# Kernel tuning notes

Measured on AMD Instinct MI355X. Metric: run time of the kernel, lower is better.

The kernel has to match this reference:

```python
import jax, jax.numpy as jnp
import numpy as np

N, M, K = 4096, 256, 32
W_EPS = 1e-6


def _spd(key, n, k):
    # well-conditioned SPD precision matrices: A A^T / k + I
    a = jax.random.normal(key, (n, k, k), dtype=jnp.float32)
    return jnp.matmul(a, jnp.swapaxes(a, -1, -2)) / k + jnp.eye(k, dtype=jnp.float32)


def setup_inputs() -> dict:
    key = jax.random.key(0)
    k1, k2, k3, k4 = jax.random.split(key, 4)
    W = jax.random.uniform(k1, (N, M), dtype=jnp.float32)
    mu_s = jax.random.normal(k2, (N, K), dtype=jnp.float32)
    omega_child = _spd(k3, N, K)
    omega_parent = _spd(k4, M, K)
    return {"W": W, "mu_s": mu_s, "omega_child": omega_child, "omega_parent": omega_parent}


def reference(W, mu_s, omega_child, omega_parent):
    # mask out negligible memberships (original skips w < 1e-6)
    wT = W.T                                   # (M, N)
    mask = wT >= W_EPS
    w = jnp.where(mask, wT, 0.0)

    # v_i = inv(omega_child_i) @ mu_s_i  -> batched solve, (N, K)
    v = jnp.linalg.solve(omega_child, mu_s[..., None])[..., 0]

    # transported means: Omega_alpha @ v_i, (M, N, K)
    T = jnp.einsum('mkl,nl->mnk', omega_parent, v)

    Z = w.sum(-1)                              # (M,)
    Zs = jnp.maximum(Z, 1e-30)
    mu_bar = jnp.einsum('mn,mnk->mk', w, T) / Zs[:, None]
    diff = T - mu_bar[:, None, :]              # (M, N, K)
    var = jnp.einsum('mn,mnk->mk', w, diff * diff) / Zs[:, None]
    psi = var.sum(-1)                          # (M,)

    # clusters with fewer than 2 contributing agents get psi = 0
    count = mask.sum(-1)
    return jnp.where(count >= 2, psi, 0.0)
```

## Files before the change

kernel.cpp:

```cpp
#include <hip/hip_runtime.h>

constexpr int N_AG = 4096;
constexpr int M_CL = 256;
constexpr int KD   = 32;
constexpr float WEPS = 1e-6f;

constexpr int PART_STRIDE = 1088;
constexpr int VT_OFF = M_CL * 4 * PART_STRIDE;
constexpr int WT_OFF = VT_OFF + N_AG * KD;

typedef __attribute__((ext_vector_type(8))) short short8;
typedef __attribute__((ext_vector_type(4))) float f32x4;

__device__ __forceinline__ float rlane(float x, int l) {
    return __int_as_float(__builtin_amdgcn_readlane(__float_as_int(x), l));
}
__device__ __forceinline__ short8 mk8(unsigned a, unsigned b, unsigned c, unsigned d) {
    union { unsigned u[4]; short8 s; } x;
    x.u[0] = a; x.u[1] = b; x.u[2] = c; x.u[3] = d;
    return x.s;
}

#define ALL32(M) M(0) M(1) M(2) M(3) M(4) M(5) M(6) M(7) \
                 M(8) M(9) M(10) M(11) M(12) M(13) M(14) M(15) \
                 M(16) M(17) M(18) M(19) M(20) M(21) M(22) M(23) \
                 M(24) M(25) M(26) M(27) M(28) M(29) M(30) M(31)

#define DECL(I) float a##I, b##I;
#define LDA(I) a##I = (c < 32) ? oc[ia_ * 1024 + I * 32 + c] : mu[ia_ * 32 + I]; \
               b##I = (c < 32) ? oc[ib_ * 1024 + I * 32 + c] : mu[ib_ * 32 + I];
#define EL(I, J) if constexpr (I != J) { \
    const float fa##I = rlane(a##I, J); a##I = fmaf(-fa##I, a##J, a##I); \
    const float fb##I = rlane(b##I, J); b##I = fmaf(-fb##I, b##J, b##I); }
#define ELALL(J) EL(0,J) EL(1,J) EL(2,J) EL(3,J) EL(4,J) EL(5,J) EL(6,J) EL(7,J) \
                 EL(8,J) EL(9,J) EL(10,J) EL(11,J) EL(12,J) EL(13,J) EL(14,J) EL(15,J) \
                 EL(16,J) EL(17,J) EL(18,J) EL(19,J) EL(20,J) EL(21,J) EL(22,J) EL(23,J) \
                 EL(24,J) EL(25,J) EL(26,J) EL(27,J) EL(28,J) EL(29,J) EL(30,J) EL(31,J)
#define STEP(J) { \
    const float pa = rlane(a##J, J); const float pb = rlane(b##J, J); \
    const float qa = 1.0f / pa;      const float qb = 1.0f / pb; \
    a##J *= qa;                      b##J *= qb; \
    ELALL(J) }
#define OUTP(I) { const float xa = rlane(a##I, 32); const float xb = rlane(b##I, 32); \
    if (lane == I) { ova = xa; ovb = xb; } }

__global__ __launch_bounds__(256, 1) void solve_transpose_kernel(
        const float* __restrict__ oc, const float* __restrict__ mu,
        const float* __restrict__ W,
        float* __restrict__ vT, float* __restrict__ Wt) {
    __shared__ float res8[32][8];
    __shared__ float tb[32][33];

    const int t    = threadIdx.x;
    const int lane = t & 63;
    const int wv   = t >> 6;
    const int idx0 = blockIdx.x * 8;
    const int ia_  = idx0 + 2 * wv;
    const int ib_  = ia_ + 1;
    const int c = (lane < 32) ? lane : 32;

    ALL32(DECL)
    ALL32(LDA)
    ALL32(STEP)

    float ova = 0.0f, ovb = 0.0f;
    ALL32(OUTP)

    if (lane < 32) {
        res8[lane][2 * wv]     = ova;
        res8[lane][2 * wv + 1] = ovb;
    }
    __syncthreads();
    {
        const int k = t >> 3, j = t & 7;
        vT[(size_t)k * 4096 + idx0 + j] = res8[k][j];
    }

    const int x = t & 31, y = t >> 5;
    #pragma unroll
    for (int rep = 0; rep < 2; ++rep) {
        const int tile = blockIdx.x * 2 + rep;
        const int n0 = (tile & 127) * 32;
        const int m0 = (tile >> 7) * 32;
        __syncthreads();
        #pragma unroll
        for (int r = 0; r < 4; ++r) {
            const int n = y + 8 * r;
            const float w = W[(size_t)(n0 + n) * 256 + m0 + x];
            tb[n][x] = (w >= WEPS) ? w : 0.0f;
        }
        __syncthreads();
        #pragma unroll
        for (int r = 0; r < 4; ++r) {
            const int mm = y + 8 * r;
            Wt[(size_t)(m0 + mm) * 4096 + n0 + x] = tb[x][mm];
        }
    }
}

__global__ __launch_bounds__(256, 4) void partial_kernel(const float* __restrict__ Wt,
                                                         const float* __restrict__ vT,
                                                         float* __restrict__ wsout) {
    const int m = blockIdx.x >> 2;
    const int p = blockIdx.x & 3;
    const int t = threadIdx.x;
    const int lane = t & 63;
    const int wv   = t >> 6;

    __shared__ float swbuf[1024];
    __shared__ float sred[4 * 1024];
    __shared__ float red[256];
    __shared__ float s1buf[32];

    const float4 wv4 = reinterpret_cast<const float4*>(Wt + (size_t)m * 4096 + p * 1024)[t];
    const float zacc = wv4.x + wv4.y + wv4.z + wv4.w;
    const float cacc = (wv4.x >= WEPS ? 1.f : 0.f) + (wv4.y >= WEPS ? 1.f : 0.f)
                     + (wv4.z >= WEPS ? 1.f : 0.f) + (wv4.w >= WEPS ? 1.f : 0.f);
    reinterpret_cast<float4*>(swbuf)[t] =
        make_float4(sqrtf(wv4.x), sqrtf(wv4.y), sqrtf(wv4.z), sqrtf(wv4.w));
    if (t < 32) s1buf[t] = 0.0f;
    __syncthreads();

    const int a = lane & 15;
    const int g = lane >> 4;
    const int nl = wv * 256 + g * 8;

    const float4* pa4 = reinterpret_cast<const float4*>(vT + (size_t)a * 4096 + p * 1024 + nl);
    const float4* pb4 = reinterpret_cast<const float4*>(vT + (size_t)(a + 16) * 4096 + p * 1024 + nl);

    f32x4 Chh[4], Chl[4];
    #pragma unroll
    for (int q = 0; q < 4; ++q) {
        Chh[q] = (f32x4){0.f, 0.f, 0.f, 0.f};
        Chl[q] = (f32x4){0.f, 0.f, 0.f, 0.f};
    }
    float s1a = 0.0f, s1b = 0.0f;

    #pragma unroll 2
    for (int ch = 0; ch < 8; ++ch) {
        const float4 va0 = pa4[ch * 8];
        const float4 va1 = pa4[ch * 8 + 1];
        const float4 vb0 = pb4[ch * 8];
        const float4 vb1 = pb4[ch * 8 + 1];
        const float4 s0  = *reinterpret_cast<const float4*>(&swbuf[nl + ch * 32]);
        const float4 s1v = *reinterpret_cast<const float4*>(&swbuf[nl + ch * 32 + 4]);

        const float ua0 = va0.x * s0.x,  ua1 = va0.y * s0.y;
        const float ua2 = va0.z * s0.z,  ua3 = va0.w * s0.w;
        const float ua4 = va1.x * s1v.x, ua5 = va1.y * s1v.y;
        const float ua6 = va1.z * s1v.z, ua7 = va1.w * s1v.w;
        const float ub0 = vb0.x * s0.x,  ub1 = vb0.y * s0.y;
        const float ub2 = vb0.z * s0.z,  ub3 = vb0.w * s0.w;
        const float ub4 = vb1.x * s1v.x, ub5 = vb1.y * s1v.y;
        const float ub6 = vb1.z * s1v.z, ub7 = vb1.w * s1v.w;

        s1a += s0.x*ua0 + s0.y*ua1 + s0.z*ua2 + s0.w*ua3
             + s1v.x*ua4 + s1v.y*ua5 + s1v.z*ua6 + s1v.w*ua7;
        s1b += s0.x*ub0 + s0.y*ub1 + s0.z*ub2 + s0.w*ub3
             + s1v.x*ub4 + s1v.y*ub5 + s1v.z*ub6 + s1v.w*ub7;

        #define BITS(u) __float_as_uint(u)
        #define LOF(u) ((u) - __uint_as_float(BITS(u) & 0xFFFF0000u))
        const short8 h0 = mk8(
            __builtin_amdgcn_perm(BITS(ua1), BITS(ua0), 0x07060302u),
            __builtin_amdgcn_perm(BITS(ua3), BITS(ua2), 0x07060302u),
            __builtin_amdgcn_perm(BITS(ua5), BITS(ua4), 0x07060302u),
            __builtin_amdgcn_perm(BITS(ua7), BITS(ua6), 0x07060302u));
        const short8 h1 = mk8(
            __builtin_amdgcn_perm(BITS(ub1), BITS(ub0), 0x07060302u),
            __builtin_amdgcn_perm(BITS(ub3), BITS(ub2), 0x07060302u),
            __builtin_amdgcn_perm(BITS(ub5), BITS(ub4), 0x07060302u),
            __builtin_amdgcn_perm(BITS(ub7), BITS(ub6), 0x07060302u));
        const float la0 = LOF(ua0), la1 = LOF(ua1), la2 = LOF(ua2), la3 = LOF(ua3);
        const float la4 = LOF(ua4), la5 = LOF(ua5), la6 = LOF(ua6), la7 = LOF(ua7);
        const float lb0 = LOF(ub0), lb1 = LOF(ub1), lb2 = LOF(ub2), lb3 = LOF(ub3);
        const float lb4 = LOF(ub4), lb5 = LOF(ub5), lb6 = LOF(ub6), lb7 = LOF(ub7);
        const short8 l0 = mk8(
            __builtin_amdgcn_perm(BITS(la1), BITS(la0), 0x07060302u),
            __builtin_amdgcn_perm(BITS(la3), BITS(la2), 0x07060302u),
            __builtin_amdgcn_perm(BITS(la5), BITS(la4), 0x07060302u),
            __builtin_amdgcn_perm(BITS(la7), BITS(la6), 0x07060302u));
        const short8 l1 = mk8(
            __builtin_amdgcn_perm(BITS(lb1), BITS(lb0), 0x07060302u),
            __builtin_amdgcn_perm(BITS(lb3), BITS(lb2), 0x07060302u),
            __builtin_amdgcn_perm(BITS(lb5), BITS(lb4), 0x07060302u),
            __builtin_amdgcn_perm(BITS(lb7), BITS(lb6), 0x07060302u));
        #undef BITS
        #undef LOF

        Chh[0] = __builtin_amdgcn_mfma_f32_16x16x32_bf16(h0, h0, Chh[0], 0, 0, 0);
        Chh[1] = __builtin_amdgcn_mfma_f32_16x16x32_bf16(h0, h1, Chh[1], 0, 0, 0);
        Chh[2] = __builtin_amdgcn_mfma_f32_16x16x32_bf16(h1, h0, Chh[2], 0, 0, 0);
        Chh[3] = __builtin_amdgcn_mfma_f32_16x16x32_bf16(h1, h1, Chh[3], 0, 0, 0);
        Chl[0] = __builtin_amdgcn_mfma_f32_16x16x32_bf16(h0, l0, Chl[0], 0, 0, 0);
        Chl[1] = __builtin_amdgcn_mfma_f32_16x16x32_bf16(h0, l1, Chl[1], 0, 0, 0);
        Chl[2] = __builtin_amdgcn_mfma_f32_16x16x32_bf16(h1, l0, Chl[2], 0, 0, 0);
        Chl[3] = __builtin_amdgcn_mfma_f32_16x16x32_bf16(h1, l1, Chl[3], 0, 0, 0);
    }

    s1a += __shfl_xor(s1a, 16); s1a += __shfl_xor(s1a, 32);
    s1b += __shfl_xor(s1b, 16); s1b += __shfl_xor(s1b, 32);
    if (lane < 16) {
        atomicAdd(&s1buf[a], s1a);
        atomicAdd(&s1buf[a + 16], s1b);
    }

    float* rw = &sred[wv * 1024];
    #pragma unroll
    for (int q = 0; q < 4; ++q) {
        const int I = q >> 1, J = q & 1;
        #pragma unroll
        for (int r = 0; r < 4; ++r) {
            const int ar = I * 16 + (lane >> 4) * 4 + r;
            const int br = J * 16 + (lane & 15);
            rw[ar * 32 + br] = Chh[q][r] + Chl[q][r];
        }
    }
    __syncthreads();
    #pragma unroll
    for (int q = 0; q < 4; ++q) {
        const int I = q >> 1, J = q & 1;
        #pragma unroll
        for (int r = 0; r < 4; ++r) {
            const int ar = I * 16 + (lane >> 4) * 4 + r;
            const int br = J * 16 + (lane & 15);
            rw[br * 32 + ar] += Chl[q][r];
        }
    }
    __syncthreads();

    const size_t base = (size_t)(m * 4 + p) * PART_STRIDE;
    float o0 = 0.f, o1 = 0.f, o2 = 0.f, o3 = 0.f;
    #pragma unroll
    for (int ww = 0; ww < 4; ++ww) {
        const float4 x = *reinterpret_cast<const float4*>(&sred[ww * 1024 + t * 4]);
        o0 += x.x; o1 += x.y; o2 += x.z; o3 += x.w;
    }
    *reinterpret_cast<float4*>(&wsout[base + t * 4]) = make_float4(o0, o1, o2, o3);

    red[t] = zacc; __syncthreads();
    #pragma unroll
    for (int s = 128; s > 0; s >>= 1) {
        if (t < s) red[t] += red[t + s];
        __syncthreads();
    }
    if (t == 0) wsout[base + 1056] = red[0];
    __syncthreads();
    red[t] = cacc; __syncthreads();
    #pragma unroll
    for (int s = 128; s > 0; s >>= 1) {
        if (t < s) red[t] += red[t + s];
        __syncthreads();
    }
    if (t == 0) wsout[base + 1057] = red[0];
    if (t < 32) wsout[base + 1024 + t] = s1buf[t];
}

__global__ __launch_bounds__(256) void combine_kernel(const float* __restrict__ op,
                                                      const float* __restrict__ ws,
                                                      float* __restrict__ out) {
    const int m = blockIdx.x;
    const int t = threadIdx.x;

    __shared__ float omg[32 * 33];
    __shared__ float vbar[32];
    __shared__ float red[256];

    #pragma unroll
    for (int i = 0; i < 4; ++i) {
        const int g = t + 256 * i;
        const int r = g >> 5, cc = g & 31;
        omg[r * 33 + cc] = op[(size_t)m * 1024 + g];
    }

    const size_t mb = (size_t)m * 4 * PART_STRIDE;
    float Z = 0.0f, cnt = 0.0f, s1 = 0.0f;
    float s2[4] = {0.f, 0.f, 0.f, 0.f};
    #pragma unroll
    for (int p2 = 0; p2 < 4; ++p2) {
        const size_t bp = mb + (size_t)p2 * PART_STRIDE;
        Z   += ws[bp + 1056];
        cnt += ws[bp + 1057];
        if (t < 32) s1 += ws[bp + 1024 + t];
        const float4 sp = *reinterpret_cast<const float4*>(&ws[bp + t * 4]);
        s2[0] += sp.x; s2[1] += sp.y; s2[2] += sp.z; s2[3] += sp.w;
    }
    const float invZ = 1.0f / fmaxf(Z, 1e-30f);
    if (t < 32) vbar[t] = s1 * invZ;
    __syncthreads();

    const int k  = t >> 3;
    const int l0 = (t & 7) * 4;
    float G[4] = {0.f, 0.f, 0.f, 0.f};
    #pragma unroll
    for (int i = 0; i < 32; ++i) {
        const float ok = omg[i * 33 + k];
        #pragma unroll
        for (int q = 0; q < 4; ++q) G[q] = fmaf(ok, omg[i * 33 + l0 + q], G[q]);
    }

    const float vk = vbar[k];
    float val = 0.0f;
    #pragma unroll
    for (int q = 0; q < 4; ++q)
        val += G[q] * (s2[q] * invZ - vk * vbar[l0 + q]);

    red[t] = val; __syncthreads();
    #pragma unroll
    for (int s = 128; s > 0; s >>= 1) {
        if (t < s) red[t] += red[t + s];
        __syncthreads();
    }
    if (t == 0) out[m] = (cnt >= 1.5f) ? red[0] : 0.0f;
}

extern "C" void kernel_launch(void* const* d_in, const int* in_sizes, int n_in,
                              void* d_out, int out_size, void* d_ws, size_t ws_size,
                              hipStream_t stream) {
    const float* W  = (const float*)d_in[0];
    const float* mu = (const float*)d_in[1];
    const float* oc = (const float*)d_in[2];
    const float* op = (const float*)d_in[3];
    float* out = (float*)d_out;
    float* ws  = (float*)d_ws;

    solve_transpose_kernel<<<512, 256, 0, stream>>>(oc, mu, W, ws + VT_OFF, ws + WT_OFF);
    partial_kernel<<<1024, 256, 0, stream>>>(ws + WT_OFF, ws + VT_OFF, ws);
    combine_kernel<<<256, 256, 0, stream>>>(op, ws, out);
}
```

Measured before the change: 116.5 us.

## Solve one system per wavefront with two lanes per row, doubling grid

Reworks the batched Gauss-Jordan solve so each wavefront handles one 32x32 system laid out row-major, two lanes per row, 16 columns each. Previously each wave handled two systems column-wise with readlane broadcasts. Loads become vectorized float4 reads, and the grid doubles to 1024 blocks, with one transpose tile per block instead of two. The aim is better coalescing, more parallelism and fewer serial readlane chains, at the cost of cross-lane shuffles and more blocks.

```diff
diff --git a/kernel.cpp b/kernel.cpp
--- a/kernel.cpp
+++ b/kernel.cpp
@@ -21,80 +21,88 @@
     return x.s;
 }
 
-#define ALL32(M) M(0) M(1) M(2) M(3) M(4) M(5) M(6) M(7) \
-                 M(8) M(9) M(10) M(11) M(12) M(13) M(14) M(15) \
-                 M(16) M(17) M(18) M(19) M(20) M(21) M(22) M(23) \
-                 M(24) M(25) M(26) M(27) M(28) M(29) M(30) M(31)
-
-#define DECL(I) float a##I, b##I;
-#define LDA(I) a##I = (c < 32) ? oc[ia_ * 1024 + I * 32 + c] : mu[ia_ * 32 + I]; \
-               b##I = (c < 32) ? oc[ib_ * 1024 + I * 32 + c] : mu[ib_ * 32 + I];
-#define EL(I, J) if constexpr (I != J) { \
-    const float fa##I = rlane(a##I, J); a##I = fmaf(-fa##I, a##J, a##I); \
-    const float fb##I = rlane(b##I, J); b##I = fmaf(-fb##I, b##J, b##I); }
-#define ELALL(J) EL(0,J) EL(1,J) EL(2,J) EL(3,J) EL(4,J) EL(5,J) EL(6,J) EL(7,J) \
-                 EL(8,J) EL(9,J) EL(10,J) EL(11,J) EL(12,J) EL(13,J) EL(14,J) EL(15,J) \
-                 EL(16,J) EL(17,J) EL(18,J) EL(19,J) EL(20,J) EL(21,J) EL(22,J) EL(23,J) \
-                 EL(24,J) EL(25,J) EL(26,J) EL(27,J) EL(28,J) EL(29,J) EL(30,J) EL(31,J)
-#define STEP(J) { \
-    const float pa = rlane(a##J, J); const float pb = rlane(b##J, J); \
-    const float qa = 1.0f / pa;      const float qb = 1.0f / pb; \
-    a##J *= qa;                      b##J *= qb; \
-    ELALL(J) }
-#define OUTP(I) { const float xa = rlane(a##I, 32); const float xb = rlane(b##I, 32); \
-    if (lane == I) { ova = xa; ovb = xb; } }
+#define ALL16(M) M(0) M(1) M(2) M(3) M(4) M(5) M(6) M(7) \
+                 M(8) M(9) M(10) M(11) M(12) M(13) M(14) M(15)
+
+#define DECLE(S) float e##S;
+#define RJ(S)    const float rA##S = rlane(e##S, LA); const float rB##S = rlane(e##S, LB);
+#define ELIM(S)  e##S = fmaf(-frA, rA##S, fmaf(-frB, rB##S, e##S));
+#define PFIX(S)  e##S = par ? rB##S * rp : rA##S * rp;
+
+#define STEP(J, S, H) { \
+    enum { LA = 2 * (J), LB = 2 * (J) + 1 }; \
+    ALL16(RJ) \
+    const float p  = rlane(e##S, 2 * (J) + (H)); \
+    const float rp = 1.0f / p; \
+    const float bn = rlane(bv, 2 * (J)) * rp; \
+    const float fs = e##S; \
+    const float fsib = __shfl_xor(fs, 1); \
+    const float f  = (par == (H)) ? fs : fsib; \
+    const float fr = f * rp; \
+    const float frA = par ? 0.0f : fr; \
+    const float frB = fr - frA; \
+    ALL16(ELIM) \
+    bv = fmaf(-f, bn, bv); \
+    if (row == (J)) { ALL16(PFIX) bv = bn; } \
+}
 
 __global__ __launch_bounds__(256, 1) void solve_transpose_kernel(
         const float* __restrict__ oc, const float* __restrict__ mu,
         const float* __restrict__ W,
         float* __restrict__ vT, float* __restrict__ Wt) {
-    __shared__ float res8[32][8];
+    __shared__ float res4[32][4];
     __shared__ float tb[32][33];
 
     const int t    = threadIdx.x;
     const int lane = t & 63;
     const int wv   = t >> 6;
-    const int idx0 = blockIdx.x * 8;
-    const int ia_  = idx0 + 2 * wv;
-    const int ib_  = ia_ + 1;
-    const int c = (lane < 32) ? lane : 32;
-
-    ALL32(DECL)
-    ALL32(LDA)
-    ALL32(STEP)
-
-    float ova = 0.0f, ovb = 0.0f;
-    ALL32(OUTP)
-
-    if (lane < 32) {
-        res8[lane][2 * wv]     = ova;
-        res8[lane][2 * wv + 1] = ovb;
-    }
-    __syncthreads();
+    const int idx  = blockIdx.x * 4 + wv;
+    const int row  = lane >> 1;
+    const int par  = lane & 1;
+
+    ALL16(DECLE)
     {
-        const int k = t >> 3, j = t & 7;
-        vT[(size_t)k * 4096 + idx0 + j] = res8[k][j];
+        const float4* src = reinterpret_cast<const float4*>(
+            oc + (size_t)idx * 1024 + row * 32 + par * 16);
+        const float4 q0 = src[0], q1 = src[1], q2 = src[2], q3 = src[3];
+        e0 = q0.x;  e1 = q0.y;  e2 = q0.z;  e3 = q0.w;
+        e4 = q1.x;  e5 = q1.y;  e6 = q1.z;  e7 = q1.w;
+        e8 = q2.x;  e9 = q2.y;  e10 = q2.z; e11 = q2.w;
+        e12 = q3.x; e13 = q3.y; e14 = q3.z; e15 = q3.w;
+    }
+    float bv = mu[(size_t)idx * 32 + row];
+
+    STEP(0,0,0)   STEP(1,1,0)   STEP(2,2,0)   STEP(3,3,0)
+    STEP(4,4,0)   STEP(5,5,0)   STEP(6,6,0)   STEP(7,7,0)
+    STEP(8,8,0)   STEP(9,9,0)   STEP(10,10,0) STEP(11,11,0)
+    STEP(12,12,0) STEP(13,13,0) STEP(14,14,0) STEP(15,15,0)
+    STEP(16,0,1)  STEP(17,1,1)  STEP(18,2,1)  STEP(19,3,1)
+    STEP(20,4,1)  STEP(21,5,1)  STEP(22,6,1)  STEP(23,7,1)
+    STEP(24,8,1)  STEP(25,9,1)  STEP(26,10,1) STEP(27,11,1)
+    STEP(28,12,1) STEP(29,13,1) STEP(30,14,1) STEP(31,15,1)
+
+    if (par == 0) res4[row][wv] = bv;
+    __syncthreads();
+    if (t < 128) {
+        const int k = t >> 2, j = t & 3;
+        vT[(size_t)k * 4096 + blockIdx.x * 4 + j] = res4[k][j];
     }
 
     const int x = t & 31, y = t >> 5;
-    #pragma unroll
-    for (int rep = 0; rep < 2; ++rep) {
-        const int tile = blockIdx.x * 2 + rep;
-        const int n0 = (tile & 127) * 32;
-        const int m0 = (tile >> 7) * 32;
-        __syncthreads();
-        #pragma unroll
-        for (int r = 0; r < 4; ++r) {
-            const int n = y + 8 * r;
-            const float w = W[(size_t)(n0 + n) * 256 + m0 + x];
-            tb[n][x] = (w >= WEPS) ? w : 0.0f;
-        }
-        __syncthreads();
-        #pragma unroll
-        for (int r = 0; r < 4; ++r) {
-            const int mm = y + 8 * r;
-            Wt[(size_t)(m0 + mm) * 4096 + n0 + x] = tb[x][mm];
-        }
+    const int tile = blockIdx.x;
+    const int n0 = (tile & 127) * 32;
+    const int m0 = (tile >> 7) * 32;
+    #pragma unroll
+    for (int r = 0; r < 4; ++r) {
+        const int n = y + 8 * r;
+        const float w = W[(size_t)(n0 + n) * 256 + m0 + x];
+        tb[n][x] = (w >= WEPS) ? w : 0.0f;
+    }
+    __syncthreads();
+    #pragma unroll
+    for (int r = 0; r < 4; ++r) {
+        const int mm = y + 8 * r;
+        Wt[(size_t)(m0 + mm) * 4096 + n0 + x] = tb[x][mm];
     }
 }
 
@@ -324,7 +332,7 @@
     float* out = (float*)d_out;
     float* ws  = (float*)d_ws;
 
-    solve_transpose_kernel<<<512, 256, 0, stream>>>(oc, mu, W, ws + VT_OFF, ws + WT_OFF);
+    solve_transpose_kernel<<<1024, 256, 0, stream>>>(oc, mu, W, ws + VT_OFF, ws + WT_OFF);
     partial_kernel<<<1024, 256, 0, stream>>>(ws + WT_OFF, ws + VT_OFF, ws);
     combine_kernel<<<256, 256, 0, stream>>>(op, ws, out);
 }
```

After: 120.9 us. 1.04x slower.
